# Optimization experiments

Hardware: AMD Instinct MI355X
Metric: run time of the kernel (lower is better)

Reference implementation:

```python
import jax, jax.numpy as jnp
import numpy as np

N = 33554432  # number of elements


def setup_inputs() -> dict:
    key = jax.random.key(0)
    kx, ky = jax.random.split(key)
    # probabilities strictly inside (0,1) so log is finite, matching intended use
    x = jax.random.uniform(kx, (N,), dtype=jnp.float32, minval=1e-6, maxval=1.0 - 1e-6)
    y = jax.random.randint(ky, (N,), 0, 2, dtype=jnp.int32)
    weights = jnp.array([0.3, 0.7], dtype=jnp.float32)  # [w_neg, w_pos]
    return {"x": x, "y": y, "weights": weights}


def reference(x, y, weights):
    # per-element: y==1 -> -log(x)*w1 ; else -> -log(1-x)*w0 ; then mean
    loss = jnp.where(y == 1, -jnp.log(x) * weights[1], -jnp.log(1.0 - x) * weights[0])
    return jnp.sum(loss) / x.shape[0]
```

## Files before the change

### kernel.cpp

```cpp
#include <hip/hip_runtime.h>


#define WBCE_BLOCK 256
#define WBCE_GRID  2048
#define WBCE_STRIDE (WBCE_GRID * WBCE_BLOCK)
#define WBCE_ITERS 16

typedef float fx4 __attribute__((ext_vector_type(4)));
typedef int   ix4 __attribute__((ext_vector_type(4)));

__device__ __forceinline__ float wbce_elem(float x, int y, float lw0, float lw1) {
    float t  = (y == 1) ? x : (1.0f - x);
    float lw = (y == 1) ? lw1 : lw0;
    return lw * __log2f(t);
}

__device__ __forceinline__ float wbce_quad(fx4 xv, ix4 yv, float lw0, float lw1) {
    float a = wbce_elem(xv.x, yv.x, lw0, lw1);
    float b = wbce_elem(xv.y, yv.y, lw0, lw1);
    float c = wbce_elem(xv.z, yv.z, lw0, lw1);
    float d = wbce_elem(xv.w, yv.w, lw0, lw1);
    return (a + b) + (c + d);
}

__global__ __launch_bounds__(WBCE_BLOCK) void weightedBCE_75582834475452_kernel(
    const fx4* __restrict__ x4,
    const ix4* __restrict__ y4,
    const float* __restrict__ weights,
    float*       __restrict__ out,
    int n4, int n, float inv_n)
{
    const float ln2 = 0.69314718055994530942f;
    const float lw0 = weights[0] * ln2;
    const float lw1 = weights[1] * ln2;

    float acc = 0.0f;
    const int tid = blockIdx.x * WBCE_BLOCK + threadIdx.x;

    if (n4 == WBCE_ITERS * WBCE_STRIDE) {
        #pragma unroll
        for (int g = 0; g < WBCE_ITERS / 4; ++g) {
            const int base = tid + g * 4 * WBCE_STRIDE;
            fx4 xa = __builtin_nontemporal_load(&x4[base + 0 * WBCE_STRIDE]);
            fx4 xb = __builtin_nontemporal_load(&x4[base + 1 * WBCE_STRIDE]);
            fx4 xc = __builtin_nontemporal_load(&x4[base + 2 * WBCE_STRIDE]);
            fx4 xd = __builtin_nontemporal_load(&x4[base + 3 * WBCE_STRIDE]);
            ix4 ya = __builtin_nontemporal_load(&y4[base + 0 * WBCE_STRIDE]);
            ix4 yb = __builtin_nontemporal_load(&y4[base + 1 * WBCE_STRIDE]);
            ix4 yc = __builtin_nontemporal_load(&y4[base + 2 * WBCE_STRIDE]);
            ix4 yd = __builtin_nontemporal_load(&y4[base + 3 * WBCE_STRIDE]);
            acc += wbce_quad(xa, ya, lw0, lw1);
            acc += wbce_quad(xb, yb, lw0, lw1);
            acc += wbce_quad(xc, yc, lw0, lw1);
            acc += wbce_quad(xd, yd, lw0, lw1);
        }
    } else {
        for (int i = tid; i < n4; i += WBCE_STRIDE) {
            fx4 xv = __builtin_nontemporal_load(&x4[i]);
            ix4 yv = __builtin_nontemporal_load(&y4[i]);
            acc += wbce_quad(xv, yv, lw0, lw1);
        }
        const float* xs = (const float*)x4;
        const int*   ys = (const int*)y4;
        for (int i = n4 * 4 + tid; i < n; i += WBCE_STRIDE) {
            acc += wbce_elem(xs[i], ys[i], lw0, lw1);
        }
    }

    #pragma unroll
    for (int off = 32; off > 0; off >>= 1)
        acc += __shfl_down(acc, off, 64);

    __shared__ float smem[WBCE_BLOCK / 64];
    const int lane = threadIdx.x & 63;
    const int wave = threadIdx.x >> 6;
    if (lane == 0) smem[wave] = acc;
    __syncthreads();

    if (threadIdx.x == 0) {
        float total = 0.0f;
        #pragma unroll
        for (int w = 0; w < WBCE_BLOCK / 64; ++w) total += smem[w];
        atomicAdd(out, -total * inv_n);
    }
}

extern "C" void kernel_launch(void* const* d_in, const int* in_sizes, int n_in,
                              void* d_out, int out_size, void* d_ws, size_t ws_size,
                              hipStream_t stream) {
    const float* x = (const float*)d_in[0];
    const int*   y = (const int*)d_in[1];
    const float* w = (const float*)d_in[2];
    float* out = (float*)d_out;
    const int n  = in_sizes[0];
    const int n4 = n >> 2;

    (void)hipMemsetAsync(out, 0, sizeof(float), stream);

    weightedBCE_75582834475452_kernel<<<WBCE_GRID, WBCE_BLOCK, 0, stream>>>(
        (const fx4*)x, (const ix4*)y, w, out, n4, n, 1.0f / (float)n);
}
```

Measured before the change: 257.6 us.

## Stream inputs through LDS with double-buffered global_load_lds prefetch

Replaces the unrolled batch of nontemporal register loads with a per-wave double-buffered pipeline. Each step issues 16-byte global_load_lds transfers straight into shared memory for the next stride, waits with an explicit vmcnt, then reads the current buffer from LDS. The aim is to overlap memory latency with compute without holding many vector registers. In exchange only one load pair is in flight per step instead of four, and every element takes an extra LDS round trip. There is also no explicit LDS wait or barrier before the shared-memory reads.

```diff
diff --git a/kernel.cpp b/kernel.cpp
--- a/kernel.cpp
+++ b/kernel.cpp
@@ -23,6 +23,13 @@
     return (a + b) + (c + d);
 }
 
+__device__ __forceinline__ void wbce_gll16(const void* g, void* l) {
+    __builtin_amdgcn_global_load_lds(
+        (const __attribute__((address_space(1))) void*)g,
+        (__attribute__((address_space(3))) void*)l,
+        16, 0, 2);
+}
+
 __global__ __launch_bounds__(WBCE_BLOCK) void weightedBCE_75582834475452_kernel(
     const fx4* __restrict__ x4,
     const ix4* __restrict__ y4,
@@ -37,22 +44,29 @@
     float acc = 0.0f;
     const int tid = blockIdx.x * WBCE_BLOCK + threadIdx.x;
 
+    __shared__ fx4 sx[WBCE_BLOCK / 64][2][64];
+    __shared__ ix4 sy[WBCE_BLOCK / 64][2][64];
+
     if (n4 == WBCE_ITERS * WBCE_STRIDE) {
+        const int wave = threadIdx.x >> 6;
+        const int lane = threadIdx.x & 63;
+
+        wbce_gll16(&x4[tid], &sx[wave][0][0]);
+        wbce_gll16(&y4[tid], &sy[wave][0][0]);
+
         #pragma unroll
-        for (int g = 0; g < WBCE_ITERS / 4; ++g) {
-            const int base = tid + g * 4 * WBCE_STRIDE;
-            fx4 xa = __builtin_nontemporal_load(&x4[base + 0 * WBCE_STRIDE]);
-            fx4 xb = __builtin_nontemporal_load(&x4[base + 1 * WBCE_STRIDE]);
-            fx4 xc = __builtin_nontemporal_load(&x4[base + 2 * WBCE_STRIDE]);
-            fx4 xd = __builtin_nontemporal_load(&x4[base + 3 * WBCE_STRIDE]);
-            ix4 ya = __builtin_nontemporal_load(&y4[base + 0 * WBCE_STRIDE]);
-            ix4 yb = __builtin_nontemporal_load(&y4[base + 1 * WBCE_STRIDE]);
-            ix4 yc = __builtin_nontemporal_load(&y4[base + 2 * WBCE_STRIDE]);
-            ix4 yd = __builtin_nontemporal_load(&y4[base + 3 * WBCE_STRIDE]);
-            acc += wbce_quad(xa, ya, lw0, lw1);
-            acc += wbce_quad(xb, yb, lw0, lw1);
-            acc += wbce_quad(xc, yc, lw0, lw1);
-            acc += wbce_quad(xd, yd, lw0, lw1);
+        for (int i = 0; i < WBCE_ITERS; ++i) {
+            const int cur = i & 1;
+            if (i + 1 < WBCE_ITERS) {
+                wbce_gll16(&x4[tid + (i + 1) * WBCE_STRIDE], &sx[wave][cur ^ 1][0]);
+                wbce_gll16(&y4[tid + (i + 1) * WBCE_STRIDE], &sy[wave][cur ^ 1][0]);
+                asm volatile("s_waitcnt vmcnt(2)" ::: "memory");
+            } else {
+                asm volatile("s_waitcnt vmcnt(0)" ::: "memory");
+            }
+            fx4 xv = sx[wave][cur][lane];
+            ix4 yv = sy[wave][cur][lane];
+            acc += wbce_quad(xv, yv, lw0, lw1);
         }
     } else {
         for (int i = tid; i < n4; i += WBCE_STRIDE) {
```

Measured after the change: 263.5 us. 1.02x slower.

## Prefetch next iteration's lines via no-op atomic compare-swap per wave

Applied to the files above, without the earlier changes.

Replaces the four-at-a-time batched loads with a one-iteration-at-a-time loop. In each iteration, 16 lanes per wave issue global_atomic_cmpswap instructions on the next iteration's x and y cache lines, using compare values chosen so they never match, which pulls those lines in as a software prefetch. The intent is to overlap the DRAM fetch with computation while keeping fewer loads in flight per thread. Atomics on streaming data can serialize at L2, add extra traffic, and lose the memory-level parallelism that the batched loads provided.

```diff
diff --git a/kernel.cpp b/kernel.cpp
--- a/kernel.cpp
+++ b/kernel.cpp
@@ -8,6 +8,7 @@
 
 typedef float fx4 __attribute__((ext_vector_type(4)));
 typedef int   ix4 __attribute__((ext_vector_type(4)));
+typedef unsigned int ux2 __attribute__((ext_vector_type(2)));
 
 __device__ __forceinline__ float wbce_elem(float x, int y, float lw0, float lw1) {
     float t  = (y == 1) ? x : (1.0f - x);
@@ -35,24 +36,29 @@
     const float lw1 = weights[1] * ln2;
 
     float acc = 0.0f;
-    const int tid = blockIdx.x * WBCE_BLOCK + threadIdx.x;
+    const int tid  = blockIdx.x * WBCE_BLOCK + threadIdx.x;
+    const int lane = threadIdx.x & 63;
 
     if (n4 == WBCE_ITERS * WBCE_STRIDE) {
         #pragma unroll
-        for (int g = 0; g < WBCE_ITERS / 4; ++g) {
-            const int base = tid + g * 4 * WBCE_STRIDE;
-            fx4 xa = __builtin_nontemporal_load(&x4[base + 0 * WBCE_STRIDE]);
-            fx4 xb = __builtin_nontemporal_load(&x4[base + 1 * WBCE_STRIDE]);
-            fx4 xc = __builtin_nontemporal_load(&x4[base + 2 * WBCE_STRIDE]);
-            fx4 xd = __builtin_nontemporal_load(&x4[base + 3 * WBCE_STRIDE]);
-            ix4 ya = __builtin_nontemporal_load(&y4[base + 0 * WBCE_STRIDE]);
-            ix4 yb = __builtin_nontemporal_load(&y4[base + 1 * WBCE_STRIDE]);
-            ix4 yc = __builtin_nontemporal_load(&y4[base + 2 * WBCE_STRIDE]);
-            ix4 yd = __builtin_nontemporal_load(&y4[base + 3 * WBCE_STRIDE]);
-            acc += wbce_quad(xa, ya, lw0, lw1);
-            acc += wbce_quad(xb, yb, lw0, lw1);
-            acc += wbce_quad(xc, yc, lw0, lw1);
-            acc += wbce_quad(xd, yd, lw0, lw1);
+        for (int i = 0; i < WBCE_ITERS; ++i) {
+            const int base = tid + i * WBCE_STRIDE;
+            fx4 xq = __builtin_nontemporal_load(&x4[base]);
+            ix4 yq = __builtin_nontemporal_load(&y4[base]);
+
+            if (i + 1 < WBCE_ITERS && lane < 16) {
+                const size_t boff =
+                    ((size_t)(tid - lane) + (size_t)(i + 1) * WBCE_STRIDE) * 16u;
+                const char* p = (lane < 8)
+                    ? ((const char*)x4 + boff + (size_t)lane * 128u)
+                    : ((const char*)y4 + boff + (size_t)(lane - 8) * 128u);
+                const unsigned cmpv = (lane < 8) ? 0x40000000u : 2u;
+                ux2 dc; dc.x = cmpv; dc.y = cmpv;
+                asm volatile("global_atomic_cmpswap %0, %1, off"
+                             :: "v"(p), "v"(dc));
+            }
+
+            acc += wbce_quad(xq, yq, lw0, lw1);
         }
     } else {
         for (int i = tid; i < n4; i += WBCE_STRIDE) {
@@ -72,7 +78,6 @@
         acc += __shfl_down(acc, off, 64);
 
     __shared__ float smem[WBCE_BLOCK / 64];
-    const int lane = threadIdx.x & 63;
     const int wave = threadIdx.x >> 6;
     if (lane == 0) smem[wave] = acc;
     __syncthreads();
```

New measurement: 355.5 us. +38.0%, slower.
